# Kernel tuning notes

Measured on AMD Instinct MI355X. Metric: run time of the kernel, lower is better.

Reference implementation:

```python
import jax, jax.numpy as jnp
import numpy as np

K = 16          # buckets per codeblock (2**treeDepth)
DEPTH = 4       # tree depth
C = 256         # codeblockCount
IN_FEATURES = 4096
OUT_FEATURES = 4096
N_ROWS = 4096

_BASE_TREE = np.array([
    [-1,-1,0,-1,0,0,0,-1,0,0,0,0,0,0,0],[-1,-1,0,-1,0,0,0,1,0,0,0,0,0,0,0],
    [-1,-1,0,1,0,0,0,0,-1,0,0,0,0,0,0],[-1,-1,0,1,0,0,0,0,1,0,0,0,0,0,0],
    [-1,1,0,0,-1,0,0,0,0,-1,0,0,0,0,0],[-1,1,0,0,-1,0,0,0,0,1,0,0,0,0,0],
    [-1,1,0,0,1,0,0,0,0,0,-1,0,0,0,0],[-1,1,0,0,1,0,0,0,0,0,1,0,0,0,0],
    [1,0,-1,0,0,-1,0,0,0,0,0,-1,0,0,0],[1,0,-1,0,0,-1,0,0,0,0,0,1,0,0,0],
    [1,0,-1,0,0,1,0,0,0,0,0,0,-1,0,0],[1,0,-1,0,0,1,0,0,0,0,0,0,1,0,0],
    [1,0,1,0,0,0,-1,0,0,0,0,0,0,-1,0],[1,0,1,0,0,0,-1,0,0,0,0,0,0,1,0],
    [1,0,1,0,0,0,1,0,0,0,0,0,0,0,-1],[1,0,1,0,0,0,1,0,0,0,0,0,0,0,1]],
    dtype=np.float32)

def _make_tree_des_matrix(c):
    # NOTE: original code initializes with ONES, then overwrites diagonal blocks
    m = np.ones((c * K, c * (K - 1)), dtype=np.float32)
    for i in range(c):
        m[i*K:(i+1)*K, i*(K-1):(i+1)*(K-1)] = _BASE_TREE
    return m

def _make_selection_matrix(c):
    base = np.zeros((K - 1, DEPTH), dtype=np.float32)
    base[0, 0] = 1.0
    for i in range(1, K - 1):
        base[i, int(np.log2(i + 1))] = 1.0
    m = np.zeros((c * (K - 1), c * DEPTH), dtype=np.float32)
    for i in range(c):
        m[i*(K-1):(i+1)*(K-1), i*DEPTH:(i+1)*DEPTH] = base
    return m

def setup_inputs() -> dict:
    key = jax.random.key(0)
    k1, k2, k3, k4 = jax.random.split(key, 4)
    inputMatrix = jax.random.normal(k1, (N_ROWS, IN_FEATURES), dtype=jnp.float32)
    dims = jax.random.randint(k2, (C * DEPTH,), 0, IN_FEATURES)
    selection_matrix = jnp.asarray(_make_selection_matrix(C))
    thresholds = jax.random.normal(k3, (C * (K - 1), 1), dtype=jnp.float32)
    tree_des_mat = jnp.asarray(_make_tree_des_matrix(C))
    lut = jax.random.normal(k4, (OUT_FEATURES, C, K), dtype=jnp.float32)
    return {"inputMatrix": inputMatrix, "dims": dims,
            "selection_matrix": selection_matrix, "thresholds": thresholds,
            "tree_des_mat": tree_des_mat, "lut": lut}

def reference(inputMatrix, dims, selection_matrix, thresholds, tree_des_mat, lut):
    n = inputMatrix.shape[0]
    c = lut.shape[1]
    # gather the tree-split feature dims: (N, C*DEPTH)
    chosen = inputMatrix[:, dims]
    # (C*15, N)
    subtracted = selection_matrix @ chosen.T - thresholds
    tanh_h = jnp.tanh(subtracted)
    sign_ste = jnp.sign(subtracted) - jax.lax.stop_gradient(tanh_h) + tanh_h
    # (C*16, N) -> (N, C, 16)
    tree_result = (tree_des_mat @ sign_ste).T.reshape(n, c, K)
    encoding_soft = jax.nn.softmax(tree_result, axis=2)
    index = jnp.argmax(encoding_soft, axis=2)
    encoding_hard = jax.nn.one_hot(index, K, dtype=encoding_soft.dtype)
    Encoded = encoding_hard - jax.lax.stop_gradient(encoding_soft) + encoding_soft
    # LUT lookup: einsum 'nij,kij->nki' + sum over i, fused to 'nij,kij->nk'
    out = jnp.einsum('nij,kij->nk', Encoded, lut)
    return out
```

## Files before the change

### kernel.cpp

```cpp
#include <hip/hip_runtime.h>

#define N_ROWS 4096
#define IN_F   4096
#define OUT_F  4096
#define C_CB   256
#define KDIM   4096

typedef short bf16x8 __attribute__((ext_vector_type(8)));
typedef float f32x4  __attribute__((ext_vector_type(4)));

union ABFrag { unsigned long long u[2]; bf16x8 v; };

__device__ __forceinline__ unsigned int f2bf(float f) {
    unsigned int u = __builtin_bit_cast(unsigned int, f);
    return (u + 0x7FFFu + ((u >> 16) & 1u)) >> 16;
}

#define CVT_BLOCKS ((OUT_F * KDIM) / (256 * 8))

__global__ void k_prep(const float* __restrict__ input, const int* __restrict__ dims,
                       const float* __restrict__ thr, unsigned char* __restrict__ idx4,
                       const float* __restrict__ lut, unsigned short* __restrict__ lutb) {
    const int b = blockIdx.x;
    if (b < N_ROWS) {
        const int n = b;
        const int c = threadIdx.x;
        const float* row = input + (size_t)n * IN_F;
        int4 d = *(const int4*)(dims + c * 4);
        const float* th = thr + c * 15;
        float x0 = row[d.x], x1 = row[d.y], x2 = row[d.z], x3 = row[d.w];
        int b0 = x0 > th[0];
        int j1 = 1 + b0;
        int b1 = x1 > th[j1];
        int j2 = 2 * j1 + 1 + b1;
        int b2 = x2 > th[j2];
        int j3 = 2 * j2 + 1 + b2;
        int b3 = x3 > th[j3];
        int idx = (b0 << 3) | (b1 << 2) | (b2 << 1) | b3;
        int other = __shfl_xor(idx, 1);
        if (!(c & 1))
            idx4[(c >> 1) * N_ROWS + n] = (unsigned char)(idx | (other << 4));
    } else {
        const int i = ((b - N_ROWS) * 256 + threadIdx.x) * 8;
        float4 a = *(const float4*)(lut + i);
        float4 f = *(const float4*)(lut + i + 4);
        uint4 o;
        o.x = f2bf(a.x) | (f2bf(a.y) << 16);
        o.y = f2bf(a.z) | (f2bf(a.w) << 16);
        o.z = f2bf(f.x) | (f2bf(f.y) << 16);
        o.w = f2bf(f.z) | (f2bf(f.w) << 16);
        *(uint4*)(lutb + i) = o;
    }
}

#define BM 128
#define BN 128
#define BKT 64
#define BSTAGE (BN * BKT * 2)
#define NT (KDIM / BKT)

template<bool STAGE_FP32>
__global__ __launch_bounds__(256, 3) void k_gemm(const unsigned short* __restrict__ lutb,
                                                 const float* __restrict__ lutf,
                                                 const unsigned char* __restrict__ idx4,
                                                 float* __restrict__ out) {
    __shared__ unsigned char smem[16384 + 2 * BSTAGE];
    unsigned char* ish  = smem;
    unsigned char* bsh0 = smem + 16384;
    unsigned char* bsh1 = smem + 16384 + BSTAGE;

    const int t   = threadIdx.x;
    const int l15 = t & 15;
    const int q   = (t >> 4) & 3;
    const int w   = t >> 6;
    const int wm  = w >> 1, wn = w & 1;

    const int bid = blockIdx.x;
    const int bx  = ((bid & 7) << 2) | ((bid >> 3) & 3);
    const int by  = bid >> 5;
    const int m0  = by * BM;
    const int n0  = bx * BN;

    #pragma unroll
    for (int qq = 0; qq < 4; qq++) {
        int L = qq * 256 + t;
        const unsigned char* g = idx4 + (size_t)(L >> 3) * N_ROWS + m0 + (L & 7) * 16;
        __builtin_amdgcn_global_load_lds(
            (const __attribute__((address_space(1))) void*)g,
            (__attribute__((address_space(3))) void*)(ish + L * 16), 16, 0, 0);
    }

    auto stageB = [&](unsigned char* dst, int kbn) {
        #pragma unroll
        for (int qq = 0; qq < 4; qq++) {
            int L = qq * 256 + t;
            int r = L >> 3, p = L & 7;
            int c = p ^ (r & 7);
            const unsigned short* g = lutb + (size_t)(n0 + r) * KDIM + kbn + c * 8;
            __builtin_amdgcn_global_load_lds(
                (const __attribute__((address_space(1))) void*)g,
                (__attribute__((address_space(3))) void*)(dst + L * 16), 16, 0, 0);
        }
    };
    auto stageB32 = [&](unsigned char* dst, int kbn) {
        #pragma unroll
        for (int qq = 0; qq < 4; qq++) {
            int L = qq * 256 + t;
            int r = L >> 3, p = L & 7;
            int c = p ^ (r & 7);
            const float* g = lutf + (size_t)(n0 + r) * KDIM + kbn + c * 8;
            float4 f0 = *(const float4*)g;
            float4 f1 = *(const float4*)(g + 4);
            uint4 o;
            o.x = f2bf(f0.x) | (f2bf(f0.y) << 16);
            o.y = f2bf(f0.z) | (f2bf(f0.w) << 16);
            o.z = f2bf(f1.x) | (f2bf(f1.y) << 16);
            o.w = f2bf(f1.z) | (f2bf(f1.w) << 16);
            *(uint4*)(dst + L * 16) = o;
        }
    };

    f32x4 acc[4][4];
    #pragma unroll
    for (int mi = 0; mi < 4; mi++)
        #pragma unroll
        for (int ni = 0; ni < 4; ni++)
            acc[mi][ni] = (f32x4){0.f, 0.f, 0.f, 0.f};

    const int xorv = l15 & 7;
    const int bRowByte = (wn * 64 + l15) * (BKT * 2);
    const int aByte = wm * 64 + l15 * 4;
    const int qh4  = (q >> 1) * 4;
    const unsigned int sub8 = (q & 1) << 3;

    auto mfmaTile = [&](const unsigned char* src, int kb) {
        ABFrag bf2[2][4];
        unsigned int w32v[2];
        #pragma unroll
        for (int s = 0; s < 2; s++) {
            const int chunkOff = ((s * 4 + q) ^ xorv) * 16;
            #pragma unroll
            for (int ni = 0; ni < 4; ni++)
                bf2[s][ni].v = *(const bf16x8*)(src + bRowByte + ni * (16 * BKT * 2) + chunkOff);
            w32v[s] = *(const unsigned int*)(ish + ((kb >> 5) + s) * 128 + aByte);
        }
        return [=](f32x4 (&ac)[4][4]) {
            #pragma unroll
            for (int s = 0; s < 2; s++) {
                ABFrag af[4];
                #pragma unroll
                for (int mi = 0; mi < 4; mi++) {
                    unsigned int T = (w32v[s] >> (mi * 8 + qh4)) & 0xFu;
                    unsigned int rel = T - sub8;
                    unsigned long long sh = 0x3F80ull << ((rel & 3) << 4);
                    af[mi].u[0] = (rel < 4u) ? sh : 0ull;
                    af[mi].u[1] = ((rel - 4u) < 4u) ? sh : 0ull;
                }
                #pragma unroll
                for (int mi = 0; mi < 4; mi++)
                    #pragma unroll
                    for (int ni = 0; ni < 4; ni++)
                        ac[mi][ni] = __builtin_amdgcn_mfma_f32_16x16x32_bf16(
                            af[mi].v, bf2[s][ni].v, ac[mi][ni], 0, 0, 0);
            }
        };
    };

    if (!STAGE_FP32) {
        stageB(bsh0, 0);
        stageB(bsh1, BKT);
        asm volatile("s_waitcnt vmcnt(4)" ::: "memory");
        __builtin_amdgcn_s_barrier();
        __builtin_amdgcn_sched_barrier(0);

        unsigned char* cur = bsh0;
        unsigned char* nxt = bsh1;
        for (int tt = 0; tt < NT; tt++) {
            const int kb = tt * BKT;
            auto doMfma = mfmaTile(cur, kb);
            asm volatile("s_waitcnt lgkmcnt(0)" ::: "memory");
            __builtin_amdgcn_s_barrier();
            __builtin_amdgcn_sched_barrier(0);
            if (tt + 2 < NT) {
                stageB(cur, kb + 2 * BKT);
                __builtin_amdgcn_sched_barrier(0);
            }
            __builtin_amdgcn_s_setprio(1);
            doMfma(acc);
            __builtin_amdgcn_s_setprio(0);
            if (tt + 2 < NT) asm volatile("s_waitcnt vmcnt(4)" ::: "memory");
            else             asm volatile("s_waitcnt vmcnt(0)" ::: "memory");
            __builtin_amdgcn_s_barrier();
            __builtin_amdgcn_sched_barrier(0);
            unsigned char* tmp = cur; cur = nxt; nxt = tmp;
        }
    } else {
        asm volatile("s_waitcnt vmcnt(0)" ::: "memory");
        __syncthreads();
        for (int tt = 0; tt < NT; tt++) {
            const int kb = tt * BKT;
            stageB32(bsh0, kb);
            __syncthreads();
            auto doMfma = mfmaTile(bsh0, kb);
            doMfma(acc);
            __syncthreads();
        }
    }

    #pragma unroll
    for (int mi = 0; mi < 4; mi++) {
        #pragma unroll
        for (int ni = 0; ni < 4; ni++) {
            const int col = n0 + wn * 64 + ni * 16 + l15;
            #pragma unroll
            for (int r = 0; r < 4; r++) {
                const int row = m0 + wm * 64 + 4 * (q * 4 + r) + mi;
                out[(size_t)row * OUT_F + col] = acc[mi][ni][r];
            }
        }
    }
}

extern "C" void kernel_launch(void* const* d_in, const int* in_sizes, int n_in,
                              void* d_out, int out_size, void* d_ws, size_t ws_size,
                              hipStream_t stream) {
    const float* input = (const float*)d_in[0];
    const int*   dims  = (const int*)d_in[1];
    const float* thr   = (const float*)d_in[3];
    const float* lut   = (const float*)d_in[5];
    float* out = (float*)d_out;

    const size_t lutbBytes = (size_t)OUT_F * KDIM * 2;
    const size_t idxBytes  = (size_t)(C_CB / 2) * N_ROWS;

    const int nblocks = (OUT_F / BN) * (N_ROWS / BM);

    if (ws_size >= lutbBytes + idxBytes) {
        unsigned short* lutb = (unsigned short*)d_ws;
        unsigned char*  idx4 = (unsigned char*)d_ws + lutbBytes;
        k_prep<<<N_ROWS + CVT_BLOCKS, 256, 0, stream>>>(input, dims, thr, idx4, lut, lutb);
        k_gemm<false><<<nblocks, 256, 0, stream>>>(lutb, lut, idx4, out);
    } else {
        unsigned char* idx4 = (unsigned char*)d_ws;
        k_prep<<<N_ROWS, 256, 0, stream>>>(input, dims, thr, idx4, lut, nullptr);
        k_gemm<true><<<nblocks, 256, 0, stream>>>(nullptr, lut, idx4, out);
    }
}
```

Measured before the change: 304.5 us.

## Halve GEMM index LDS footprint via two-phase staging to raise occupancy

The GEMM now keeps only half of the per-block code-index tile in LDS at a time, reloading the second half midway through the K loop. This cuts the LDS allocation so the launch bound can rise from 3 to 4 blocks per CU, giving more latency hiding. The prep kernel is split into a separate index kernel, which first stages the input row and thresholds into LDS with coalesced loads, and a separate LUT-to-bf16 conversion kernel. The risks are register spills under the tighter launch bound, an extra kernel launch, and the index kernel now reading every full input row.

New measurement: 297.4 us. 1.02x faster.

```diff
diff --git a/kernel.cpp b/kernel.cpp
--- a/kernel.cpp
+++ b/kernel.cpp
@@ -16,41 +16,55 @@
     return (u + 0x7FFFu + ((u >> 16) & 1u)) >> 16;
 }
 
-#define CVT_BLOCKS ((OUT_F * KDIM) / (256 * 8))
-
-__global__ void k_prep(const float* __restrict__ input, const int* __restrict__ dims,
-                       const float* __restrict__ thr, unsigned char* __restrict__ idx4,
-                       const float* __restrict__ lut, unsigned short* __restrict__ lutb) {
-    const int b = blockIdx.x;
-    if (b < N_ROWS) {
-        const int n = b;
-        const int c = threadIdx.x;
-        const float* row = input + (size_t)n * IN_F;
-        int4 d = *(const int4*)(dims + c * 4);
-        const float* th = thr + c * 15;
-        float x0 = row[d.x], x1 = row[d.y], x2 = row[d.z], x3 = row[d.w];
-        int b0 = x0 > th[0];
-        int j1 = 1 + b0;
-        int b1 = x1 > th[j1];
-        int j2 = 2 * j1 + 1 + b1;
-        int b2 = x2 > th[j2];
-        int j3 = 2 * j2 + 1 + b2;
-        int b3 = x3 > th[j3];
-        int idx = (b0 << 3) | (b1 << 2) | (b2 << 1) | b3;
-        int other = __shfl_xor(idx, 1);
-        if (!(c & 1))
-            idx4[(c >> 1) * N_ROWS + n] = (unsigned char)(idx | (other << 4));
-    } else {
-        const int i = ((b - N_ROWS) * 256 + threadIdx.x) * 8;
-        float4 a = *(const float4*)(lut + i);
-        float4 f = *(const float4*)(lut + i + 4);
-        uint4 o;
-        o.x = f2bf(a.x) | (f2bf(a.y) << 16);
-        o.y = f2bf(a.z) | (f2bf(a.w) << 16);
-        o.z = f2bf(f.x) | (f2bf(f.y) << 16);
-        o.w = f2bf(f.z) | (f2bf(f.w) << 16);
-        *(uint4*)(lutb + i) = o;
-    }
+__global__ __launch_bounds__(256) void k_idx(const float* __restrict__ input,
+                                             const int* __restrict__ dims,
+                                             const float* __restrict__ thr,
+                                             unsigned char* __restrict__ idx4) {
+    __shared__ float rowS[IN_F];
+    __shared__ float thrS[C_CB * 15];
+    __shared__ int   dimS[C_CB * 4];
+    const int n = blockIdx.x;
+    const int t = threadIdx.x;
+
+    #pragma unroll
+    for (int i = 0; i < 4; i++) dimS[i * 256 + t] = dims[i * 256 + t];
+    #pragma unroll
+    for (int i = 0; i < 15; i++) thrS[i * 256 + t] = thr[i * 256 + t];
+    const float* row = input + (size_t)n * IN_F;
+    #pragma unroll
+    for (int i = 0; i < 4; i++) {
+        float4 v = *(const float4*)(row + i * 1024 + t * 4);
+        *(float4*)(rowS + i * 1024 + t * 4) = v;
+    }
+    __syncthreads();
+
+    const int c = t;
+    int4 d = *(const int4*)(dimS + c * 4);
+    const float* th = thrS + c * 15;
+    float x0 = rowS[d.x], x1 = rowS[d.y], x2 = rowS[d.z], x3 = rowS[d.w];
+    int b0 = x0 > th[0];
+    int j1 = 1 + b0;
+    int b1 = x1 > th[j1];
+    int j2 = 2 * j1 + 1 + b1;
+    int b2 = x2 > th[j2];
+    int j3 = 2 * j2 + 1 + b2;
+    int b3 = x3 > th[j3];
+    int idx = (b0 << 3) | (b1 << 2) | (b2 << 1) | b3;
+    int other = __shfl_xor(idx, 1);
+    if (!(c & 1))
+        idx4[(c >> 1) * N_ROWS + n] = (unsigned char)(idx | (other << 4));
+}
+
+__global__ void k_cvt(const float* __restrict__ lut, unsigned short* __restrict__ lutb) {
+    const int i = (blockIdx.x * blockDim.x + threadIdx.x) * 8;
+    float4 a = *(const float4*)(lut + i);
+    float4 b = *(const float4*)(lut + i + 4);
+    uint4 o;
+    o.x = f2bf(a.x) | (f2bf(a.y) << 16);
+    o.y = f2bf(a.z) | (f2bf(a.w) << 16);
+    o.z = f2bf(b.x) | (f2bf(b.y) << 16);
+    o.w = f2bf(b.z) | (f2bf(b.w) << 16);
+    *(uint4*)(lutb + i) = o;
 }
 
 #define BM 128
@@ -60,14 +74,14 @@
 #define NT (KDIM / BKT)
 
 template<bool STAGE_FP32>
-__global__ __launch_bounds__(256, 3) void k_gemm(const unsigned short* __restrict__ lutb,
+__global__ __launch_bounds__(256, 4) void k_gemm(const unsigned short* __restrict__ lutb,
                                                  const float* __restrict__ lutf,
                                                  const unsigned char* __restrict__ idx4,
                                                  float* __restrict__ out) {
-    __shared__ unsigned char smem[16384 + 2 * BSTAGE];
+    __shared__ unsigned char smem[8192 + 2 * BSTAGE];
     unsigned char* ish  = smem;
-    unsigned char* bsh0 = smem + 16384;
-    unsigned char* bsh1 = smem + 16384 + BSTAGE;
+    unsigned char* bsh0 = smem + 8192;
+    unsigned char* bsh1 = smem + 8192 + BSTAGE;
 
     const int t   = threadIdx.x;
     const int l15 = t & 15;
@@ -81,14 +95,16 @@
     const int m0  = by * BM;
     const int n0  = bx * BN;
 
-    #pragma unroll
-    for (int qq = 0; qq < 4; qq++) {
-        int L = qq * 256 + t;
-        const unsigned char* g = idx4 + (size_t)(L >> 3) * N_ROWS + m0 + (L & 7) * 16;
-        __builtin_amdgcn_global_load_lds(
-            (const __attribute__((address_space(1))) void*)g,
-            (__attribute__((address_space(3))) void*)(ish + L * 16), 16, 0, 0);
-    }
+    auto stageIdx = [&](int h) {
+        #pragma unroll
+        for (int qq = 0; qq < 2; qq++) {
+            int L = qq * 256 + t;
+            const unsigned char* g = idx4 + (size_t)(h * 64 + (L >> 3)) * N_ROWS + m0 + (L & 7) * 16;
+            __builtin_amdgcn_global_load_lds(
+                (const __attribute__((address_space(1))) void*)g,
+                (__attribute__((address_space(3))) void*)(ish + L * 16), 16, 0, 0);
+        }
+    };
 
     auto stageB = [&](unsigned char* dst, int kbn) {
         #pragma unroll
@@ -142,7 +158,7 @@
             #pragma unroll
             for (int ni = 0; ni < 4; ni++)
                 bf2[s][ni].v = *(const bf16x8*)(src + bRowByte + ni * (16 * BKT * 2) + chunkOff);
-            w32v[s] = *(const unsigned int*)(ish + ((kb >> 5) + s) * 128 + aByte);
+            w32v[s] = *(const unsigned int*)(ish + ((((kb >> 5) + s) & 63) * 128) + aByte);
         }
         return [=](f32x4 (&ac)[4][4]) {
             #pragma unroll
@@ -167,6 +183,7 @@
     };
 
     if (!STAGE_FP32) {
+        stageIdx(0);
         stageB(bsh0, 0);
         stageB(bsh1, BKT);
         asm volatile("s_waitcnt vmcnt(4)" ::: "memory");
@@ -181,10 +198,9 @@
             asm volatile("s_waitcnt lgkmcnt(0)" ::: "memory");
             __builtin_amdgcn_s_barrier();
             __builtin_amdgcn_sched_barrier(0);
-            if (tt + 2 < NT) {
-                stageB(cur, kb + 2 * BKT);
-                __builtin_amdgcn_sched_barrier(0);
-            }
+            if (tt == 31) stageIdx(1);
+            if (tt + 2 < NT) stageB(cur, kb + 2 * BKT);
+            __builtin_amdgcn_sched_barrier(0);
             __builtin_amdgcn_s_setprio(1);
             doMfma(acc);
             __builtin_amdgcn_s_setprio(0);
@@ -195,10 +211,12 @@
             unsigned char* tmp = cur; cur = nxt; nxt = tmp;
         }
     } else {
+        stageIdx(0);
         asm volatile("s_waitcnt vmcnt(0)" ::: "memory");
         __syncthreads();
         for (int tt = 0; tt < NT; tt++) {
             const int kb = tt * BKT;
+            if (tt == 32) stageIdx(1);
             stageB32(bsh0, kb);
             __syncthreads();
             auto doMfma = mfmaTile(bsh0, kb);
@@ -238,11 +256,12 @@
     if (ws_size >= lutbBytes + idxBytes) {
         unsigned short* lutb = (unsigned short*)d_ws;
         unsigned char*  idx4 = (unsigned char*)d_ws + lutbBytes;
-        k_prep<<<N_ROWS + CVT_BLOCKS, 256, 0, stream>>>(input, dims, thr, idx4, lut, lutb);
+        k_idx<<<N_ROWS, C_CB, 0, stream>>>(input, dims, thr, idx4);
+        k_cvt<<<(OUT_F * KDIM) / (256 * 8), 256, 0, stream>>>(lut, lutb);
         k_gemm<false><<<nblocks, 256, 0, stream>>>(lutb, lut, idx4, out);
     } else {
         unsigned char* idx4 = (unsigned char*)d_ws;
-        k_prep<<<N_ROWS, 256, 0, stream>>>(input, dims, thr, idx4, lut, nullptr);
+        k_idx<<<N_ROWS, C_CB, 0, stream>>>(input, dims, thr, idx4);
         k_gemm<true><<<nblocks, 256, 0, stream>>>(nullptr, lut, idx4, out);
     }
 }
```
